# Kernel tuning notes

Hardware: AMD Instinct MI355X
Metric: run time of the kernel (lower is better)

## Reference

```python
import jax, jax.numpy as jnp
import numpy as np

C = 256
NUM_HEADS = 8
HEAD_DIM = C // NUM_HEADS


def setup_inputs() -> dict:
    key = jax.random.key(0)
    ks = jax.random.split(key, 12)
    d = {}
    d["x"] = jax.random.normal(ks[0], (1, C, 16, 32, 32), dtype=jnp.float32)
    # temporal conv: Conv3d kernel (3,1,1) -> store as [C_out, C_in, 3]
    d["tc_w"] = jax.random.normal(ks[1], (C, C, 3), dtype=jnp.float32) * 0.02
    d["tc_b"] = jnp.zeros((C,), dtype=jnp.float32)
    # 1x1x1 conv3d projections == per-channel linear, store as [C_out, C_in]
    for i, n in enumerate(["q", "k", "v", "o"]):
        d[n + "_w"] = jax.random.normal(ks[2 + i], (C, C), dtype=jnp.float32) * 0.02
        d[n + "_b"] = jnp.zeros((C,), dtype=jnp.float32)
    # learned temporal positional embedding [1, C, 16, 1, 1]
    d["pos_emb"] = jax.random.normal(ks[10], (1, C, 16, 1, 1), dtype=jnp.float32) * 0.02
    return d


def _proj(w, b, y):
    # 1x1x1 Conv3d == channel-mixing linear on [B,C,T,H,W]
    return jnp.einsum('oc,bcthw->bothw', w, y) + b[None, :, None, None, None]


def _forward(x, tc_w, tc_b, q_w, q_b, k_w, k_b, v_w, v_b, o_w, o_b, pos_emb):
    B, Cc, T, H, W = x.shape
    nh, hd = NUM_HEADS, Cc // NUM_HEADS
    # ---- temporal_conv: Conv3d kernel (3,1,1), padding (1,0,0) ----
    x4 = x.reshape(B, Cc, T, H * W)
    local = jax.lax.conv_general_dilated(
        x4, tc_w[:, :, :, None], window_strides=(1, 1),
        padding=((1, 1), (0, 0)),
        dimension_numbers=('NCHW', 'OIHW', 'NCHW'))
    local = local.reshape(B, Cc, T, H, W) + tc_b[None, :, None, None, None]
    # ---- temporal attention (per-frame spatial attention) ----
    xp = x + pos_emb[:, :, :T]  # T <= 16, plain slice
    q = _proj(q_w, q_b, xp)
    k = _proj(k_w, k_b, xp)
    v = _proj(v_w, v_b, xp)

    def heads(y):  # [B,C,T,H,W] -> [B,nh,T,P,hd]
        return y.reshape(B, nh, hd, T, H * W).transpose(0, 1, 3, 4, 2)

    q, k, v = heads(q), heads(k), heads(v)
    scale = hd ** -0.5
    attn = jax.nn.softmax(jnp.einsum('bntpd,bntqd->bntpq', q, k) * scale, axis=-1)
    out = jnp.einsum('bntpq,bntqd->bntpd', attn, v)
    out = out.transpose(0, 1, 4, 2, 3).reshape(B, Cc, T, H, W)  # b (n d) t h w
    out = _proj(o_w, o_b, out)
    return local + out


def reference(x, tc_w, tc_b, q_w, q_b, k_w, k_b, v_w, v_b, o_w, o_b, pos_emb):
    return _forward(x, tc_w, tc_b, q_w, q_b, k_w, k_b, v_w, v_b, o_w, o_b, pos_emb)
```

## Files before the change

kernel.cpp:

```cpp
#include <hip/hip_runtime.h>
#include <hip/hip_bf16.h>


typedef __bf16 bf16x8 __attribute__((ext_vector_type(8)));
typedef float  f32x4  __attribute__((ext_vector_type(4)));

__device__ __forceinline__ ushort f2bf(float f) {
    union { float f; unsigned int u; } x; x.f = f;
    unsigned int r = x.u + 0x7FFFu + ((x.u >> 16) & 1u);
    return (ushort)(r >> 16);
}

__device__ __forceinline__ bf16x8 ldg8(const ushort* p) {
    union { int4 i; bf16x8 b; } u;
    u.i = *reinterpret_cast<const int4*>(p);
    return u.b;
}

#define SCL_QK 0.25504600765996234f

__global__ __launch_bounds__(256)
void prep_all(const float* __restrict__ x, const float* __restrict__ pos,
              const float* __restrict__ qw, const float* __restrict__ kw,
              const float* __restrict__ vw, const float* __restrict__ ow,
              const float* __restrict__ tcw,
              const float* __restrict__ qb, const float* __restrict__ kb,
              const float* __restrict__ vb, const float* __restrict__ ob,
              const float* __restrict__ tcb,
              ushort* __restrict__ xpt, ushort* __restrict__ wqkv,
              ushort* __restrict__ wfin, float* __restrict__ bqkv,
              float* __restrict__ bfin)
{
    const int b   = blockIdx.x;
    const int tid = threadIdx.x;
    if (b < 1024) {
        __shared__ float tile[64][65];
        const int tp0 = (b & 255) * 64;
        const int c0  = (b >> 8) * 64;
        const int t   = tp0 >> 10;
        {
            const int j4 = (tid & 15) * 4;
            const int i0 = tid >> 4;
            #pragma unroll
            for (int rr = 0; rr < 4; ++rr) {
                int i = rr * 16 + i0;
                float4 vv = *reinterpret_cast<const float4*>(
                    &x[(size_t)(c0 + i) * 16384 + tp0 + j4]);
                tile[i][j4 + 0] = vv.x; tile[i][j4 + 1] = vv.y;
                tile[i][j4 + 2] = vv.z; tile[i][j4 + 3] = vv.w;
            }
        }
        __syncthreads();
        {
            const int cq = (tid & 15) * 4;
            const int i0 = tid >> 4;
            float pv0 = pos[(c0 + cq + 0) * 16 + t];
            float pv1 = pos[(c0 + cq + 1) * 16 + t];
            float pv2 = pos[(c0 + cq + 2) * 16 + t];
            float pv3 = pos[(c0 + cq + 3) * 16 + t];
            #pragma unroll
            for (int rr = 0; rr < 4; ++rr) {
                int jj = rr * 16 + i0;
                ushort4 pk;
                pk.x = f2bf(tile[cq + 0][jj] + pv0);
                pk.y = f2bf(tile[cq + 1][jj] + pv1);
                pk.z = f2bf(tile[cq + 2][jj] + pv2);
                pk.w = f2bf(tile[cq + 3][jj] + pv3);
                *reinterpret_cast<ushort4*>(&xpt[(size_t)(tp0 + jj) * 256 + c0 + cq]) = pk;
            }
        }
    } else if (b < 1280) {
        __shared__ float red[256][16];
        const int o = b - 1024;
        const int c = tid;
        const float w0 = tcw[o * 768 + c * 3 + 0];
        const float w1 = tcw[o * 768 + c * 3 + 1];
        const float w2 = tcw[o * 768 + c * 3 + 2];
        float p[16];
        #pragma unroll
        for (int t = 0; t < 16; ++t) p[t] = pos[c * 16 + t];
        #pragma unroll
        for (int t = 0; t < 16; ++t) {
            float pm1 = (t > 0)  ? p[t - 1] : 0.f;
            float pp1 = (t < 15) ? p[t + 1] : 0.f;
            red[c][t] = w0 * pm1 + w1 * p[t] + w2 * pp1;
        }
        __syncthreads();
        #pragma unroll
        for (int s = 128; s >= 1; s >>= 1) {
            if (c < s)
                #pragma unroll
                for (int t = 0; t < 16; ++t) red[c][t] += red[c + s][t];
            __syncthreads();
        }
        if (c < 16) bfin[c * 256 + o] = ob[o] + tcb[o] - red[0][c];
    } else {
        int i = (b - 1280) * 256 + tid;
        if (i < 196608) {
            int m = i >> 8, k = i & 255;
            float val = (m < 256) ? qw[m * 256 + k]
                      : (m < 512) ? kw[(m - 256) * 256 + k]
                                  : vw[(m - 512) * 256 + k];
            wqkv[i] = f2bf(val);
        } else if (i < 458752) {
            int p = i - 196608;
            int o = p >> 10, col = p & 1023;
            float val;
            if (col < 256) val = ow[o * 256 + col];
            else { int q = col - 256; int c = q & 255, kseg = q >> 8;
                   val = tcw[o * 768 + c * 3 + kseg]; }
            wfin[p] = f2bf(val);
        } else if (i < 459520) {
            int bq = i - 458752;
            bqkv[bq] = (bq < 256) ? qb[bq] : (bq < 512) ? kb[bq - 256] : vb[bq - 512];
        }
    }
}

template<int MODE>
__global__ __launch_bounds__(256)
void gemm_bt(const ushort* __restrict__ A, const ushort* __restrict__ B,
             const ushort* __restrict__ B2,
             void* __restrict__ outp, void* __restrict__ outp2,
             const float* __restrict__ bias,
             const int M, const int N, const int K)
{
    __shared__ __align__(16) ushort As[128][72];
    __shared__ __align__(16) ushort Bs[64][72];

    const int tid  = threadIdx.x;
    const int lane = tid & 63;
    const int w    = tid >> 6;
    const int lr   = lane & 15;
    const int hk   = lane >> 4;

    const int n0 = blockIdx.x * 64;
    const int m0 = blockIdx.y * 128;
    const int wm = w * 32;

    const int srow = tid >> 3;
    const int scol = (tid & 7) * 8;

    f32x4 acc[2][4] = {};

    for (int kk0 = 0; kk0 < K; kk0 += 64) {
        const int seg  = kk0 >> 8;
        const int bcol = kk0 & 255;
        const ushort* bs = B;
        bool ok = true;
        if constexpr (MODE == 3) {
            if (seg != 0) {
                int tf = (n0 >> 10) + seg - 2;
                ok = ((unsigned)tf < 16u);
                bs = B2 + (((ptrdiff_t)seg - 2) << 18);
            }
        }
        __syncthreads();
        #pragma unroll
        for (int q = 0; q < 4; ++q) {
            const int row = srow + q * 32;
            *reinterpret_cast<int4*>(&As[row][scol]) =
                *reinterpret_cast<const int4*>(A + (size_t)(m0 + row) * K + kk0 + scol);
        }
        if (ok) {
            #pragma unroll
            for (int q = 0; q < 2; ++q) {
                const int row = srow + q * 32;
                *reinterpret_cast<int4*>(&Bs[row][scol]) =
                    *reinterpret_cast<const int4*>(bs + (size_t)(n0 + row) * 256 + bcol + scol);
            }
        } else {
            #pragma unroll
            for (int q = 0; q < 2; ++q)
                *reinterpret_cast<int4*>(&Bs[srow + q * 32][scol]) = make_int4(0, 0, 0, 0);
        }
        __syncthreads();
        #pragma unroll
        for (int ks = 0; ks < 2; ++ks) {
            bf16x8 af[2], bfr[4];
            #pragma unroll
            for (int mi = 0; mi < 2; ++mi)
                af[mi] = *reinterpret_cast<const bf16x8*>(&As[wm + mi * 16 + lr][ks * 32 + hk * 8]);
            #pragma unroll
            for (int nj = 0; nj < 4; ++nj)
                bfr[nj] = *reinterpret_cast<const bf16x8*>(&Bs[nj * 16 + lr][ks * 32 + hk * 8]);
            #pragma unroll
            for (int mi = 0; mi < 2; ++mi)
                #pragma unroll
                for (int nj = 0; nj < 4; ++nj)
                    acc[mi][nj] = __builtin_amdgcn_mfma_f32_16x16x32_bf16(af[mi], bfr[nj], acc[mi][nj], 0, 0, 0);
        }
    }

    const float* bb = bias;
    if constexpr (MODE == 3) bb = bias + ((n0 >> 10) << 8);

    #pragma unroll
    for (int mi = 0; mi < 2; ++mi) {
        const int mb = m0 + wm + mi * 16 + hk * 4;
        const float b0 = bb[mb + 0], b1 = bb[mb + 1], b2 = bb[mb + 2], b3 = bb[mb + 3];
        #pragma unroll
        for (int nj = 0; nj < 4; ++nj) {
            const int n = n0 + nj * 16 + lr;
            const f32x4 a = acc[mi][nj];
            if constexpr (MODE == 0) {
                if (mb < 512) {
                    const float sc = (mb < 256) ? SCL_QK : 1.0f;
                    ushort4 pk;
                    pk.x = f2bf((a[0] + b0) * sc); pk.y = f2bf((a[1] + b1) * sc);
                    pk.z = f2bf((a[2] + b2) * sc); pk.w = f2bf((a[3] + b3) * sc);
                    ushort* o = (ushort*)outp;
                    size_t base = (size_t)(mb >> 8) * (8ull * 16384 * 32)
                                + (size_t)((mb >> 5) & 7) * (16384ull * 32)
                                + (mb & 31);
                    *reinterpret_cast<ushort4*>(o + base + (size_t)n * 32) = pk;
                } else {
                    int c = mb - 512;
                    ushort* o = (ushort*)outp2;
                    o[(size_t)(c + 0) * 16384 + n] = f2bf(a[0] + b0);
                    o[(size_t)(c + 1) * 16384 + n] = f2bf(a[1] + b1);
                    o[(size_t)(c + 2) * 16384 + n] = f2bf(a[2] + b2);
                    o[(size_t)(c + 3) * 16384 + n] = f2bf(a[3] + b3);
                }
            } else {
                float* o = (float*)outp;
                o[(size_t)(mb + 0) * N + n] = a[0] + b0;
                o[(size_t)(mb + 1) * N + n] = a[1] + b1;
                o[(size_t)(mb + 2) * N + n] = a[2] + b2;
                o[(size_t)(mb + 3) * N + n] = a[3] + b3;
            }
        }
    }
}

__global__ __launch_bounds__(512, 4)
void attn_kernel(const ushort* __restrict__ qhd, const ushort* __restrict__ v,
                 ushort* __restrict__ outp)
{
    __shared__ float comb[4][24][64];

    const int tid  = threadIdx.x;
    const int lane = tid & 63;
    const int w    = tid >> 6;
    const int ws   = w & 3;
    const int kvh  = w >> 2;
    const int lr   = lane & 15;
    const int hk   = lane >> 4;

    const int prob = blockIdx.x;
    const int qb   = blockIdx.y;
    const int hn   = prob >> 4, t = prob & 15;

    const ushort* qh = qhd + (size_t)hn * (16384 * 32);
    const ushort* kh = qhd + 8ull * 16384 * 32 + (size_t)hn * (16384 * 32);

    const int p0 = qb * 128 + ws * 32;
    const size_t rowbase = (size_t)t * 1024;
    const int kv0 = kvh * 512;

    const ushort* kptr  = kh + (rowbase + kv0 + lr) * 32 + hk * 8;
    const ushort* vptr0 = v + (size_t)(hn * 32 + lr) * 16384 + rowbase + kv0 + hk * 8;
    const ushort* vptr1 = vptr0 + 262144;

    bf16x8 qf[2];
    #pragma unroll
    for (int mi = 0; mi < 2; ++mi)
        qf[mi] = ldg8(qh + (rowbase + p0 + mi * 16 + lr) * 32 + hk * 8);

    union { ushort s[8]; bf16x8 v; } onesu;
    #pragma unroll
    for (int j = 0; j < 8; ++j) onesu.s[j] = 0x3F80;
    const bf16x8 ones = onesu.v;

    f32x4 o_acc[2][2] = {};
    f32x4 lsum[2] = {};
    const f32x4 fzero = {};

    for (int it = 0; it < 8; ++it) {
        bf16x8 vf[2][2];
        vf[0][0] = ldg8(vptr0);      vf[0][1] = ldg8(vptr1);
        vf[1][0] = ldg8(vptr0 + 32); vf[1][1] = ldg8(vptr1 + 32);
        bf16x8 kf[4];
        #pragma unroll
        for (int nj = 0; nj < 4; ++nj)
            kf[nj] = ldg8(kptr + nj * 512);
        f32x4 s[4][2];
        #pragma unroll
        for (int nj = 0; nj < 4; ++nj)
            #pragma unroll
            for (int mi = 0; mi < 2; ++mi)
                s[nj][mi] = __builtin_amdgcn_mfma_f32_16x16x32_bf16(kf[nj], qf[mi], fzero, 0, 0, 0);
        uint u[2][8];
        #pragma unroll
        for (int mi = 0; mi < 2; ++mi) {
            float ps[16];
            #pragma unroll
            for (int nj = 0; nj < 4; ++nj)
                #pragma unroll
                for (int r = 0; r < 4; ++r)
                    ps[nj * 4 + r] = exp2f(s[nj][mi][r]);
            #pragma unroll
            for (int j = 0; j < 8; ++j)
                asm("v_cvt_pk_bf16_f32 %0, %1, %2" : "=v"(u[mi][j]) : "v"(ps[2 * j]), "v"(ps[2 * j + 1]));
            asm("v_permlane32_swap_b32 %0, %1" : "+v"(u[mi][0]), "+v"(u[mi][2]));
            asm("v_permlane32_swap_b32 %0, %1" : "+v"(u[mi][1]), "+v"(u[mi][3]));
            asm("v_permlane16_swap_b32 %0, %1" : "+v"(u[mi][0]), "+v"(u[mi][2]));
            asm("v_permlane16_swap_b32 %0, %1" : "+v"(u[mi][1]), "+v"(u[mi][3]));
            asm("v_permlane32_swap_b32 %0, %1" : "+v"(u[mi][4]), "+v"(u[mi][6]));
            asm("v_permlane32_swap_b32 %0, %1" : "+v"(u[mi][5]), "+v"(u[mi][7]));
            asm("v_permlane16_swap_b32 %0, %1" : "+v"(u[mi][4]), "+v"(u[mi][6]));
            asm("v_permlane16_swap_b32 %0, %1" : "+v"(u[mi][5]), "+v"(u[mi][7]));
        }
        #pragma unroll
        for (int kq = 0; kq < 2; ++kq) {
            #pragma unroll
            for (int mi = 0; mi < 2; ++mi) {
                union { uint4 i; bf16x8 b; } pu;
                pu.i = make_uint4(u[mi][kq * 4 + 0], u[mi][kq * 4 + 1],
                                  u[mi][kq * 4 + 2], u[mi][kq * 4 + 3]);
                lsum[mi] = __builtin_amdgcn_mfma_f32_16x16x32_bf16(pu.b, ones, lsum[mi], 0, 0, 0);
                o_acc[mi][0] = __builtin_amdgcn_mfma_f32_16x16x32_bf16(pu.b, vf[kq][0], o_acc[mi][0], 0, 0, 0);
                o_acc[mi][1] = __builtin_amdgcn_mfma_f32_16x16x32_bf16(pu.b, vf[kq][1], o_acc[mi][1], 0, 0, 0);
            }
        }
        kptr += 2048; vptr0 += 64; vptr1 += 64;
    }

    if (kvh == 1) {
        #pragma unroll
        for (int mi = 0; mi < 2; ++mi) {
            #pragma unroll
            for (int nf = 0; nf < 2; ++nf)
                #pragma unroll
                for (int r = 0; r < 4; ++r)
                    comb[ws][mi * 8 + nf * 4 + r][lane] = o_acc[mi][nf][r];
            #pragma unroll
            for (int r = 0; r < 4; ++r)
                comb[ws][16 + mi * 4 + r][lane] = lsum[mi][r];
        }
    }
    __syncthreads();
    if (kvh == 0) {
        #pragma unroll
        for (int mi = 0; mi < 2; ++mi) {
            #pragma unroll
            for (int nf = 0; nf < 2; ++nf)
                #pragma unroll
                for (int r = 0; r < 4; ++r)
                    o_acc[mi][nf][r] += comb[ws][mi * 8 + nf * 4 + r][lane];
            #pragma unroll
            for (int r = 0; r < 4; ++r)
                lsum[mi][r] += comb[ws][16 + mi * 4 + r][lane];
        }
        #pragma unroll
        for (int mi = 0; mi < 2; ++mi) {
            float inv[4];
            #pragma unroll
            for (int r = 0; r < 4; ++r) inv[r] = 1.f / lsum[mi][r];
            #pragma unroll
            for (int nf = 0; nf < 2; ++nf)
                #pragma unroll
                for (int r = 0; r < 4; ++r)
                    outp[(rowbase + p0 + mi * 16 + hk * 4 + r) * 256 + hn * 32 + nf * 16 + lr] =
                        f2bf(o_acc[mi][nf][r] * inv[r]);
        }
    }
}

extern "C" void kernel_launch(void* const* d_in, const int* in_sizes, int n_in,
                              void* d_out, int out_size, void* d_ws, size_t ws_size,
                              hipStream_t stream)
{
    const float* x   = (const float*)d_in[0];
    const float* tcw = (const float*)d_in[1];
    const float* tcb = (const float*)d_in[2];
    const float* qw  = (const float*)d_in[3];
    const float* qb  = (const float*)d_in[4];
    const float* kw  = (const float*)d_in[5];
    const float* kb  = (const float*)d_in[6];
    const float* vw  = (const float*)d_in[7];
    const float* vb  = (const float*)d_in[8];
    const float* ow  = (const float*)d_in[9];
    const float* ob  = (const float*)d_in[10];
    const float* pos = (const float*)d_in[11];

    char* ws = (char*)d_ws;
    size_t off = 0;
    auto alloc = [&](size_t bytes) {
        void* p = ws + off;
        off += (bytes + 255) & ~(size_t)255;
        return p;
    };
    ushort* xpt   = (ushort*)alloc(16384ull * 256 * 2);
    ushort* qkhd  = (ushort*)alloc(2ull * 8 * 16384 * 32 * 2);
    ushort* vbuf  = (ushort*)alloc(256ull * 16384 * 2);
    ushort* attnb = (ushort*)alloc(16384ull * 256 * 2);
    ushort* wqkv  = (ushort*)alloc(768ull * 256 * 2);
    ushort* wfin  = (ushort*)alloc(256ull * 1024 * 2);
    float*  bqkv  = (float*)alloc(768 * 4);
    float*  bfin  = (float*)alloc(16ull * 256 * 4);

    prep_all<<<3075, 256, 0, stream>>>(x, pos, qw, kw, vw, ow, tcw, qb, kb, vb, ob, tcb,
                                       xpt, wqkv, wfin, bqkv, bfin);

    gemm_bt<0><<<dim3(256, 6), 256, 0, stream>>>(wqkv, xpt, nullptr, qkhd, vbuf, bqkv,
                                                 768, 16384, 256);

    attn_kernel<<<dim3(128, 8), 512, 0, stream>>>(qkhd, vbuf, attnb);

    gemm_bt<3><<<dim3(256, 2), 256, 0, stream>>>(wfin, attnb, xpt, (float*)d_out, nullptr, bfin,
                                                 256, 16384, 1024);
}
```

Baseline: 104.4 us.

## Stage V-projection epilogue through LDS, stagger attention KV order, add MFMA priority

The GEMM epilogue for the V rows (m0 >= 512) now writes bf16 results into shared memory and then emits coalesced 16-byte row stores, replacing the scattered 2-byte stores. In the attention kernel each wave starts its KV loop at a different offset, (it + w) & 7, to spread memory accesses. The MFMA sections are wrapped in s_setprio so waves doing matrix math are favoured in scheduling. The staging adds two barriers and LDS traffic, and the rotated order changes the summation order of the partial sums.

```diff
diff --git a/kernel.cpp b/kernel.cpp
--- a/kernel.cpp
+++ b/kernel.cpp
@@ -192,37 +192,70 @@
         }
     }
 
-    const float* bb = bias;
-    if constexpr (MODE == 3) bb = bias + ((n0 >> 10) << 8);
-
-    #pragma unroll
-    for (int mi = 0; mi < 2; ++mi) {
-        const int mb = m0 + wm + mi * 16 + hk * 4;
-        const float b0 = bb[mb + 0], b1 = bb[mb + 1], b2 = bb[mb + 2], b3 = bb[mb + 3];
-        #pragma unroll
-        for (int nj = 0; nj < 4; ++nj) {
-            const int n = n0 + nj * 16 + lr;
-            const f32x4 a = acc[mi][nj];
-            if constexpr (MODE == 0) {
-                if (mb < 512) {
-                    const float sc = (mb < 256) ? SCL_QK : 1.0f;
-                    ushort4 pk;
-                    pk.x = f2bf((a[0] + b0) * sc); pk.y = f2bf((a[1] + b1) * sc);
-                    pk.z = f2bf((a[2] + b2) * sc); pk.w = f2bf((a[3] + b3) * sc);
-                    ushort* o = (ushort*)outp;
-                    size_t base = (size_t)(mb >> 8) * (8ull * 16384 * 32)
-                                + (size_t)((mb >> 5) & 7) * (16384ull * 32)
-                                + (mb & 31);
-                    *reinterpret_cast<ushort4*>(o + base + (size_t)n * 32) = pk;
-                } else {
-                    int c = mb - 512;
-                    ushort* o = (ushort*)outp2;
-                    o[(size_t)(c + 0) * 16384 + n] = f2bf(a[0] + b0);
-                    o[(size_t)(c + 1) * 16384 + n] = f2bf(a[1] + b1);
-                    o[(size_t)(c + 2) * 16384 + n] = f2bf(a[2] + b2);
-                    o[(size_t)(c + 3) * 16384 + n] = f2bf(a[3] + b3);
+    if constexpr (MODE == 0) {
+        if (m0 >= 512) {
+            __syncthreads();
+            #pragma unroll
+            for (int mi = 0; mi < 2; ++mi) {
+                const int mb = m0 + wm + mi * 16 + hk * 4;
+                const float b0 = bias[mb + 0], b1 = bias[mb + 1],
+                            b2 = bias[mb + 2], b3 = bias[mb + 3];
+                const int ml = wm + mi * 16 + hk * 4;
+                #pragma unroll
+                for (int nj = 0; nj < 4; ++nj) {
+                    const f32x4 a = acc[mi][nj];
+                    const int nl = nj * 16 + lr;
+                    As[ml + 0][nl] = f2bf(a[0] + b0);
+                    As[ml + 1][nl] = f2bf(a[1] + b1);
+                    As[ml + 2][nl] = f2bf(a[2] + b2);
+                    As[ml + 3][nl] = f2bf(a[3] + b3);
                 }
-            } else {
+            }
+            __syncthreads();
+            ushort* o = (ushort*)outp2;
+            const int r2 = tid >> 2, c4 = (tid & 3) * 8;
+            #pragma unroll
+            for (int rp = 0; rp < 2; ++rp)
+                #pragma unroll
+                for (int j = 0; j < 2; ++j) {
+                    const int row = rp * 64 + r2, col = j * 32 + c4;
+                    *reinterpret_cast<int4*>(
+                        &o[(size_t)(m0 - 512 + row) * 16384 + n0 + col]) =
+                        *reinterpret_cast<const int4*>(&As[row][col]);
+                }
+            return;
+        }
+        #pragma unroll
+        for (int mi = 0; mi < 2; ++mi) {
+            const int mb = m0 + wm + mi * 16 + hk * 4;
+            const float b0 = bias[mb + 0], b1 = bias[mb + 1],
+                        b2 = bias[mb + 2], b3 = bias[mb + 3];
+            const float sc = (mb < 256) ? SCL_QK : 1.0f;
+            #pragma unroll
+            for (int nj = 0; nj < 4; ++nj) {
+                const int n = n0 + nj * 16 + lr;
+                const f32x4 a = acc[mi][nj];
+                ushort4 pk;
+                pk.x = f2bf((a[0] + b0) * sc); pk.y = f2bf((a[1] + b1) * sc);
+                pk.z = f2bf((a[2] + b2) * sc); pk.w = f2bf((a[3] + b3) * sc);
+                ushort* o = (ushort*)outp;
+                size_t base = (size_t)(mb >> 8) * (8ull * 16384 * 32)
+                            + (size_t)((mb >> 5) & 7) * (16384ull * 32)
+                            + (mb & 31);
+                *reinterpret_cast<ushort4*>(o + base + (size_t)n * 32) = pk;
+            }
+        }
+    } else {
+        const float* bb = bias + ((n0 >> 10) << 8);
+        #pragma unroll
+        for (int mi = 0; mi < 2; ++mi) {
+            const int mb = m0 + wm + mi * 16 + hk * 4;
+            const float b0 = bb[mb + 0], b1 = bb[mb + 1],
+                        b2 = bb[mb + 2], b3 = bb[mb + 3];
+            #pragma unroll
+            for (int nj = 0; nj < 4; ++nj) {
+                const int n = n0 + nj * 16 + lr;
+                const f32x4 a = acc[mi][nj];
                 float* o = (float*)outp;
                 o[(size_t)(mb + 0) * N + n] = a[0] + b0;
                 o[(size_t)(mb + 1) * N + n] = a[1] + b1;
@@ -277,19 +310,25 @@
     const f32x4 fzero = {};
 
     for (int it = 0; it < 8; ++it) {
+        const int ii = (it + w) & 7;
+        const ushort* kp  = kptr  + ii * 2048;
+        const ushort* vp0 = vptr0 + ii * 64;
+        const ushort* vp1 = vptr1 + ii * 64;
         bf16x8 vf[2][2];
-        vf[0][0] = ldg8(vptr0);      vf[0][1] = ldg8(vptr1);
-        vf[1][0] = ldg8(vptr0 + 32); vf[1][1] = ldg8(vptr1 + 32);
+        vf[0][0] = ldg8(vp0);      vf[0][1] = ldg8(vp1);
+        vf[1][0] = ldg8(vp0 + 32); vf[1][1] = ldg8(vp1 + 32);
         bf16x8 kf[4];
         #pragma unroll
         for (int nj = 0; nj < 4; ++nj)
-            kf[nj] = ldg8(kptr + nj * 512);
+            kf[nj] = ldg8(kp + nj * 512);
         f32x4 s[4][2];
+        __builtin_amdgcn_s_setprio(1);
         #pragma unroll
         for (int nj = 0; nj < 4; ++nj)
             #pragma unroll
             for (int mi = 0; mi < 2; ++mi)
                 s[nj][mi] = __builtin_amdgcn_mfma_f32_16x16x32_bf16(kf[nj], qf[mi], fzero, 0, 0, 0);
+        __builtin_amdgcn_s_setprio(0);
         uint u[2][8];
         #pragma unroll
         for (int mi = 0; mi < 2; ++mi) {
@@ -311,6 +350,7 @@
             asm("v_permlane16_swap_b32 %0, %1" : "+v"(u[mi][4]), "+v"(u[mi][6]));
             asm("v_permlane16_swap_b32 %0, %1" : "+v"(u[mi][5]), "+v"(u[mi][7]));
         }
+        __builtin_amdgcn_s_setprio(1);
         #pragma unroll
         for (int kq = 0; kq < 2; ++kq) {
             #pragma unroll
@@ -323,7 +363,7 @@
                 o_acc[mi][1] = __builtin_amdgcn_mfma_f32_16x16x32_bf16(pu.b, vf[kq][1], o_acc[mi][1], 0, 0, 0);
             }
         }
-        kptr += 2048; vptr0 += 64; vptr1 += 64;
+        __builtin_amdgcn_s_setprio(0);
     }
 
     if (kvh == 1) {
```

Result: no change. 106.2 us (+1.7%).
